# Optimization experiments

Measured on AMD Instinct MI355X. Metric: run time of the kernel, lower is better.

The kernel has to match this reference:

```python
import jax, jax.numpy as jnp
import numpy as np

N_NODES = 16384
N_EDGES = 8192
MAX_DEG = 32
IN_DIM = 128
EDGE_DIM = 64
N_HEADS = 8
OUT_DIM = 16
OUT_CH = N_HEADS * OUT_DIM  # 128 == IN_DIM -> residual is Identity


def setup_inputs() -> dict:
    key = jax.random.key(0)
    ks = jax.random.split(key, 16)
    # incidence matrix H [N, E]: each hyperedge touches up to MAX_DEG random nodes
    rng = np.random.default_rng(0)
    cols = rng.integers(0, N_NODES, size=(N_EDGES, MAX_DEG))
    H_np = np.zeros((N_NODES, N_EDGES), dtype=np.float32)
    H_np[cols, np.arange(N_EDGES)[:, None]] = 1.0  # duplicates collapse -> deg <= MAX_DEG
    s = 0.02
    return {
        "q": jax.random.normal(ks[0], (N_NODES, IN_DIM), jnp.float32),
        "k": jax.random.normal(ks[1], (N_NODES, IN_DIM), jnp.float32),
        "v": jax.random.normal(ks[2], (N_NODES, IN_DIM), jnp.float32),
        "edge_feat": jax.random.normal(ks[3], (N_NODES, EDGE_DIM), jnp.float32),
        "H": jnp.asarray(H_np),
        "Wq": jax.random.normal(ks[4], (IN_DIM, OUT_CH), jnp.float32) * s,
        "Wk": jax.random.normal(ks[5], (IN_DIM, OUT_CH), jnp.float32) * s,
        "Wv": jax.random.normal(ks[6], (IN_DIM, OUT_CH), jnp.float32) * s,
        "We": jax.random.normal(ks[7], (EDGE_DIM, N_HEADS), jnp.float32) * s,
        "be": jnp.zeros((N_HEADS,), jnp.float32),
        "Wo": jax.random.normal(ks[8], (OUT_CH, OUT_CH), jnp.float32) * s,
        "W1": jax.random.normal(ks[9], (OUT_CH, 2 * OUT_CH), jnp.float32) * s,
        "b1": jnp.zeros((2 * OUT_CH,), jnp.float32),
        "W2": jax.random.normal(ks[10], (2 * OUT_CH, OUT_CH), jnp.float32) * s,
        "b2": jnp.zeros((OUT_CH,), jnp.float32),
        "max_deg": MAX_DEG,
    }


def hgt_forward(q, k, v, edge_feat, H, Wq, Wk, Wv, We, be, Wo, W1, b1, W2, b2, max_deg):
    N = q.shape[0]
    E = H.shape[1]
    nH, C = be.shape[0], Wq.shape[1]
    d = C // nH
    scale = 1.0 / (d ** 0.5)

    qd = (q @ Wq).reshape(N, nH, d)
    ksrc = (k @ Wk).reshape(N, nH, d)
    vsrc = (v @ Wv).reshape(N, nH, d)

    Ht = H.T  # [E, N]
    # node indices of each hyperedge, padded to max_deg (stable argsort: ones first, ascending)
    idx = jnp.argsort(-Ht, axis=1)[:, :max_deg]            # [E, K]
    deg = jnp.sum(Ht, axis=1).astype(jnp.int32)            # [E]
    mask = jnp.arange(max_deg)[None, :] < deg[:, None]     # [E, K]

    q_pad = qd[idx]   # [E, K, nH, d]
    k_pad = ksrc[idx]
    score = jnp.sum(q_pad * k_pad, axis=-1) * scale        # [E, K, nH]

    # hyperedge features and ADD edge attention bias
    he_feat = Ht @ edge_feat                               # [E, edge_dim]
    edge_attn = he_feat @ We + be                          # [E, nH]
    score = score + edge_attn[:, None, :]

    # segment softmax over nodes (normalize each node's attention over its hyperedges)
    flat_idx = jnp.where(mask, idx, N).reshape(-1)         # invalid slots -> dummy segment N
    score_flat = jnp.where(mask[..., None], score, -jnp.inf).reshape(-1, nH)
    seg_max = jax.ops.segment_max(score_flat, flat_idx, num_segments=N + 1)[:N]  # [N, nH]
    exp_e = jnp.where(mask[..., None], jnp.exp(score - seg_max[idx]), 0.0)       # [E, K, nH]
    seg_sum = jax.ops.segment_sum(exp_e.reshape(-1, nH), flat_idx, num_segments=N + 1)[:N]
    attn = exp_e / (seg_sum[idx] + 1e-10)                  # [E, K, nH]; 0 at padded slots

    # messages and aggregation: rst = H @ sum_over_slots(attn * v)
    v_pad = vsrc[idx]                                      # [E, K, nH, d]
    msg_sum = jnp.sum((v_pad * attn[..., None]).reshape(E, max_deg, C), axis=1)  # [E, C]
    rst = H @ msg_sum                                      # [N, C]

    rst = rst @ Wo
    rst = rst + q                                          # residual (Identity: in_dim == out_channel)
    h = rst
    rst = jax.nn.relu(rst @ W1 + b1) @ W2 + b2             # FFN
    return rst + h                                         # second residual


def reference(q, k, v, edge_feat, H, Wq, Wk, Wv, We, be, Wo, W1, b1, W2, b2, max_deg):
    return hgt_forward(q, k, v, edge_feat, H, Wq, Wk, Wv, We, be, Wo, W1, b1, W2, b2, max_deg)
```

## Files before the change

kernel.cpp:

```cpp
#include <hip/hip_runtime.h>

#define N_NODES 16384
#define N_EDGES 8192
#define MAXD 32
#define NODE_CAP 64

#define GEMM_BLKS 512
#define PE_BLKS 256
#define CVT_BLKS 256

typedef __attribute__((ext_vector_type(8))) short bf16x8;
typedef __attribute__((ext_vector_type(4))) float f32x4;

__device__ __forceinline__ unsigned f2b(float f) {
    unsigned u = __float_as_uint(f);
    return (u + 0x7FFFu + ((u >> 16) & 1u)) >> 16;
}
__device__ __forceinline__ unsigned pack2(float lo, float hi) {
    return f2b(lo) | (f2b(hi) << 16);
}
__device__ __forceinline__ float blo(unsigned w) { return __uint_as_float(w << 16); }
__device__ __forceinline__ float bhi(unsigned w) { return __uint_as_float(w & 0xFFFF0000u); }

__device__ __forceinline__ int row_u4(uint4 x, int c4, int row, int base,
                                      int* __restrict__ node_edges, int lane)
{
    const unsigned* xs = (const unsigned*)&x;
#pragma unroll
    for (int k2 = 0; k2 < 4; ++k2) {
        unsigned long long m = __ballot(xs[k2] != 0u);
        if (xs[k2]) {
            int pos = base + (int)__popcll(m & ((1ull << lane) - 1ull));
            if (pos < NODE_CAP) node_edges[row * NODE_CAP + pos] = c4 * 4 + k2;
        }
        base += (int)__popcll(m);
    }
    return base;
}

__global__ __launch_bounds__(256, 8) void scan_rows_k(const float* __restrict__ H,
    int* __restrict__ node_cnt, int* __restrict__ node_edges)
{
    const int wid  = threadIdx.x >> 6;
    const int lane = threadIdx.x & 63;
    const int row  = blockIdx.x * 4 + wid;
    const uint4* Hr = (const uint4*)H + (size_t)row * 2048;
    int base = 0;
#pragma unroll 1
    for (int it = 0; it < 32; it += 4) {
        uint4 x0 = Hr[(it + 0) * 64 + lane];
        uint4 x1 = Hr[(it + 1) * 64 + lane];
        uint4 x2 = Hr[(it + 2) * 64 + lane];
        uint4 x3 = Hr[(it + 3) * 64 + lane];
        base = row_u4(x0, (it + 0) * 64 + lane, row, base, node_edges, lane);
        base = row_u4(x1, (it + 1) * 64 + lane, row, base, node_edges, lane);
        base = row_u4(x2, (it + 2) * 64 + lane, row, base, node_edges, lane);
        base = row_u4(x3, (it + 3) * 64 + lane, row, base, node_edges, lane);
    }
    if (lane == 0) node_cnt[row] = base;
}

__global__ __launch_bounds__(256) void build_k(const int* __restrict__ node_cnt,
    const int* __restrict__ node_edges, int* __restrict__ edge_cnt,
    int* __restrict__ edge_nodes)
{
    int idx = blockIdx.x * 256 + threadIdx.x;
    int n = idx >> 6, s = idx & 63;
    if (s < min(node_cnt[n], NODE_CAP)) {
        int e = node_edges[n * NODE_CAP + s];
        int p = atomicAdd(&edge_cnt[e], 1);
        if (p < MAXD) edge_nodes[e * MAXD + p] = n;
    }
}

__global__ __launch_bounds__(256) void vwe_k(
    const float* __restrict__ v, const float* __restrict__ Wv,
    const float* __restrict__ ef, const float* __restrict__ We,
    const float* __restrict__ W1, const float* __restrict__ W2,
    float* __restrict__ vsrc, float* __restrict__ pe,
    unsigned short* __restrict__ W1t, unsigned short* __restrict__ W2t)
{
    const int b = blockIdx.x, tid = threadIdx.x;
    if (b < GEMM_BLKS) {
        const int row0 = b * 32;
        const int r  = tid >> 4;
        const int c0 = (tid & 15) * 8;
        const float4* A4 = (const float4*)v;
        const float4* B4 = (const float4*)Wv;
        float acc[2][8];
#pragma unroll
        for (int i = 0; i < 2; ++i)
#pragma unroll
            for (int j = 0; j < 8; ++j) acc[i][j] = 0.f;
#pragma unroll 4
        for (int k4 = 0; k4 < 32; ++k4) {
            float4 a0 = A4[(size_t)(row0 + r) * 32 + k4];
            float4 a1 = A4[(size_t)(row0 + r + 16) * 32 + k4];
#pragma unroll
            for (int kk = 0; kk < 4; ++kk) {
                int k = k4 * 4 + kk;
                float4 b0 = B4[k * 32 + (c0 >> 2)];
                float4 b1 = B4[k * 32 + (c0 >> 2) + 1];
                float av0 = kk == 0 ? a0.x : kk == 1 ? a0.y : kk == 2 ? a0.z : a0.w;
                float av1 = kk == 0 ? a1.x : kk == 1 ? a1.y : kk == 2 ? a1.z : a1.w;
                acc[0][0] = fmaf(av0, b0.x, acc[0][0]); acc[0][1] = fmaf(av0, b0.y, acc[0][1]);
                acc[0][2] = fmaf(av0, b0.z, acc[0][2]); acc[0][3] = fmaf(av0, b0.w, acc[0][3]);
                acc[0][4] = fmaf(av0, b1.x, acc[0][4]); acc[0][5] = fmaf(av0, b1.y, acc[0][5]);
                acc[0][6] = fmaf(av0, b1.z, acc[0][6]); acc[0][7] = fmaf(av0, b1.w, acc[0][7]);
                acc[1][0] = fmaf(av1, b0.x, acc[1][0]); acc[1][1] = fmaf(av1, b0.y, acc[1][1]);
                acc[1][2] = fmaf(av1, b0.z, acc[1][2]); acc[1][3] = fmaf(av1, b0.w, acc[1][3]);
                acc[1][4] = fmaf(av1, b1.x, acc[1][4]); acc[1][5] = fmaf(av1, b1.y, acc[1][5]);
                acc[1][6] = fmaf(av1, b1.z, acc[1][6]); acc[1][7] = fmaf(av1, b1.w, acc[1][7]);
            }
        }
#pragma unroll
        for (int i = 0; i < 2; ++i) {
            int row = row0 + r + i * 16;
            float4 o0 = {acc[i][0], acc[i][1], acc[i][2], acc[i][3]};
            float4 o1 = {acc[i][4], acc[i][5], acc[i][6], acc[i][7]};
            *(float4*)&vsrc[(size_t)row * 128 + c0]     = o0;
            *(float4*)&vsrc[(size_t)row * 128 + c0 + 4] = o1;
        }
    } else if (b < GEMM_BLKS + PE_BLKS) {
        int base = (b - GEMM_BLKS) * 512 + tid;
#pragma unroll
        for (int t = 0; t < 2; ++t) {
            int g = base + t * 256;
            int n = g >> 3, h = g & 7;
            const float4* ef4 = (const float4*)ef + n * 16;
            float p = 0.f;
#pragma unroll
            for (int d4 = 0; d4 < 16; ++d4) {
                float4 x = ef4[d4];
                p += x.x * We[(d4 * 4 + 0) * 8 + h] + x.y * We[(d4 * 4 + 1) * 8 + h]
                   + x.z * We[(d4 * 4 + 2) * 8 + h] + x.w * We[(d4 * 4 + 3) * 8 + h];
            }
            pe[g] = p;
        }
    } else {
        int g2 = (b - GEMM_BLKS - PE_BLKS) * 256 + tid;
        if (g2 < 32768) {
            int n = g2 >> 7, k = g2 & 127;
            W1t[g2] = (unsigned short)f2b(W1[k * 256 + n]);
        } else {
            int g3 = g2 - 32768;
            int n = g3 >> 8, k = g3 & 255;
            W2t[g3] = (unsigned short)f2b(W2[k * 128 + n]);
        }
    }
}

__global__ __launch_bounds__(256) void eexp_k(const int* __restrict__ edge_cnt,
    const int* __restrict__ edge_nodes, const float* __restrict__ pe,
    const float* __restrict__ be, float* __restrict__ eexp)
{
    int g = blockIdx.x * 256 + threadIdx.x;
    int e = g >> 3, h = g & 7;
    int cnt = min(edge_cnt[e], MAXD);
    float s0 = be[h], s1 = 0.f, s2 = 0.f, s3 = 0.f;
    int j = 0;
    for (; j + 4 <= cnt; j += 4) {
        int4 nn = *(const int4*)&edge_nodes[e * MAXD + j];
        s0 += pe[nn.x * 8 + h];
        s1 += pe[nn.y * 8 + h];
        s2 += pe[nn.z * 8 + h];
        s3 += pe[nn.w * 8 + h];
    }
    for (; j < cnt; ++j) s0 += pe[edge_nodes[e * MAXD + j] * 8 + h];
    eexp[g] = __expf((s0 + s1) + (s2 + s3));
}

__global__ __launch_bounds__(256) void zu_k(const int* __restrict__ node_cnt,
    const int* __restrict__ node_edges, const float* __restrict__ eexp,
    const float* __restrict__ vsrc, uint4* __restrict__ u4)
{
    int g = blockIdx.x * 256 + threadIdx.x;
    int n = g >> 3, h = g & 7;
    int cnt = min(node_cnt[n], NODE_CAP);
    float z0 = 0.f, z1 = 0.f, z2 = 0.f, z3 = 0.f;
    int i = 0;
    for (; i + 4 <= cnt; i += 4) {
        int4 ee = *(const int4*)&node_edges[n * NODE_CAP + i];
        z0 += eexp[ee.x * 8 + h];
        z1 += eexp[ee.y * 8 + h];
        z2 += eexp[ee.z * 8 + h];
        z3 += eexp[ee.w * 8 + h];
    }
    for (; i < cnt; ++i) z0 += eexp[node_edges[n * NODE_CAP + i] * 8 + h];
    float s = 1.0f / (((z0 + z1) + (z2 + z3)) + 1e-10f);

    const float4* v4 = (const float4*)vsrc + (size_t)n * 32 + h * 4;
    float4 x0 = v4[0], x1 = v4[1], x2 = v4[2], x3 = v4[3];
    uint4 w0, w1;
    w0.x = pack2(s * x0.x, s * x0.y); w0.y = pack2(s * x0.z, s * x0.w);
    w0.z = pack2(s * x1.x, s * x1.y); w0.w = pack2(s * x1.z, s * x1.w);
    w1.x = pack2(s * x2.x, s * x2.y); w1.y = pack2(s * x2.z, s * x2.w);
    w1.z = pack2(s * x3.x, s * x3.y); w1.w = pack2(s * x3.z, s * x3.w);
    u4[(size_t)n * 16 + h * 2]     = w0;
    u4[(size_t)n * 16 + h * 2 + 1] = w1;
}

__global__ __launch_bounds__(256) void msgwo_k(const int* __restrict__ edge_cnt,
    const int* __restrict__ edge_nodes, const float* __restrict__ eexp,
    const uint4* __restrict__ u4, const float* __restrict__ Wo,
    uint4* __restrict__ msgo4)
{
    __shared__ float Ms[16][128];
    __shared__ float Bs[32][128];
    const int tid = threadIdx.x;
    const int e0  = blockIdx.x * 16;

    {
        int le = tid >> 4, c8 = tid & 15;
        int e = e0 + le;
        int h = c8 >> 1;
        int cnt = min(edge_cnt[e], MAXD);
        float eh = eexp[e * 8 + h];
        float a[8];
#pragma unroll
        for (int k = 0; k < 8; ++k) a[k] = 0.f;
        int j = 0;
        for (; j + 4 <= cnt; j += 4) {
            int4 nn = *(const int4*)&edge_nodes[e * MAXD + j];
            uint4 w0 = u4[(size_t)nn.x * 16 + c8];
            uint4 w1 = u4[(size_t)nn.y * 16 + c8];
            uint4 w2 = u4[(size_t)nn.z * 16 + c8];
            uint4 w3 = u4[(size_t)nn.w * 16 + c8];
            a[0] += (blo(w0.x) + blo(w1.x)) + (blo(w2.x) + blo(w3.x));
            a[1] += (bhi(w0.x) + bhi(w1.x)) + (bhi(w2.x) + bhi(w3.x));
            a[2] += (blo(w0.y) + blo(w1.y)) + (blo(w2.y) + blo(w3.y));
            a[3] += (bhi(w0.y) + bhi(w1.y)) + (bhi(w2.y) + bhi(w3.y));
            a[4] += (blo(w0.z) + blo(w1.z)) + (blo(w2.z) + blo(w3.z));
            a[5] += (bhi(w0.z) + bhi(w1.z)) + (bhi(w2.z) + bhi(w3.z));
            a[6] += (blo(w0.w) + blo(w1.w)) + (blo(w2.w) + blo(w3.w));
            a[7] += (bhi(w0.w) + bhi(w1.w)) + (bhi(w2.w) + bhi(w3.w));
        }
        for (; j < cnt; ++j) {
            uint4 w = u4[(size_t)edge_nodes[e * MAXD + j] * 16 + c8];
            a[0] += blo(w.x); a[1] += bhi(w.x); a[2] += blo(w.y); a[3] += bhi(w.y);
            a[4] += blo(w.z); a[5] += bhi(w.z); a[6] += blo(w.w); a[7] += bhi(w.w);
        }
        float4 o0 = {a[0]*eh, a[1]*eh, a[2]*eh, a[3]*eh};
        float4 o1 = {a[4]*eh, a[5]*eh, a[6]*eh, a[7]*eh};
        *(float4*)&Ms[le][c8 * 8]     = o0;
        *(float4*)&Ms[le][c8 * 8 + 4] = o1;
    }
    __syncthreads();

    const int r  = tid >> 4;
    const int c0 = (tid & 15) * 8;
    float acc[8];
#pragma unroll
    for (int j = 0; j < 8; ++j) acc[j] = 0.f;

    for (int kt = 0; kt < 128; kt += 32) {
#pragma unroll
        for (int u0 = 0; u0 < 4; ++u0) {
            int u = u0 * 256 + tid;
            int kk = u >> 5, cc = (u & 31) * 4;
            *(float4*)&Bs[kk][cc] = *(const float4*)&Wo[(kt + kk) * 128 + cc];
        }
        __syncthreads();
#pragma unroll
        for (int k = 0; k < 32; ++k) {
            float a = Ms[r][kt + k];
#pragma unroll
            for (int j = 0; j < 8; ++j)
                acc[j] = fmaf(a, Bs[k][c0 + j], acc[j]);
        }
        __syncthreads();
    }
    uint4 w;
    w.x = pack2(acc[0], acc[1]); w.y = pack2(acc[2], acc[3]);
    w.z = pack2(acc[4], acc[5]); w.w = pack2(acc[6], acc[7]);
    msgo4[(size_t)(e0 + r) * 16 + (c0 >> 3)] = w;
}

__global__ __launch_bounds__(256) void ffn_agg_k(const float* __restrict__ q,
    const int* __restrict__ node_cnt, const int* __restrict__ node_edges,
    const uint4* __restrict__ msgo4, const unsigned short* __restrict__ W1t,
    const float* __restrict__ b1, const unsigned short* __restrict__ W2t,
    const float* __restrict__ b2, float* __restrict__ out)
{
    __shared__ float Hs[32][128];
    __shared__ unsigned short Ha[32][128];
    __shared__ unsigned short Ta[32][256];

    const int tid  = threadIdx.x;
    const int row0 = blockIdx.x * 32;

    {
        int r = tid >> 3, lc = tid & 7;
        int n = row0 + r;
        const float4* q4 = (const float4*)q + (size_t)n * 32 + lc * 4;
        float a[16];
        {
            float4 qa = q4[0], qb = q4[1], qc = q4[2], qd = q4[3];
            a[0]=qa.x; a[1]=qa.y; a[2]=qa.z; a[3]=qa.w;
            a[4]=qb.x; a[5]=qb.y; a[6]=qb.z; a[7]=qb.w;
            a[8]=qc.x; a[9]=qc.y; a[10]=qc.z; a[11]=qc.w;
            a[12]=qd.x; a[13]=qd.y; a[14]=qd.z; a[15]=qd.w;
        }
        int cnt = min(node_cnt[n], NODE_CAP);
        int i = 0;
        for (; i + 2 <= cnt; i += 2) {
            int ea = node_edges[n * NODE_CAP + i];
            int eb = node_edges[n * NODE_CAP + i + 1];
            uint4 wa0 = msgo4[(size_t)ea * 16 + lc * 2];
            uint4 wa1 = msgo4[(size_t)ea * 16 + lc * 2 + 1];
            uint4 wb0 = msgo4[(size_t)eb * 16 + lc * 2];
            uint4 wb1 = msgo4[(size_t)eb * 16 + lc * 2 + 1];
            a[0]  += blo(wa0.x) + blo(wb0.x); a[1]  += bhi(wa0.x) + bhi(wb0.x);
            a[2]  += blo(wa0.y) + blo(wb0.y); a[3]  += bhi(wa0.y) + bhi(wb0.y);
            a[4]  += blo(wa0.z) + blo(wb0.z); a[5]  += bhi(wa0.z) + bhi(wb0.z);
            a[6]  += blo(wa0.w) + blo(wb0.w); a[7]  += bhi(wa0.w) + bhi(wb0.w);
            a[8]  += blo(wa1.x) + blo(wb1.x); a[9]  += bhi(wa1.x) + bhi(wb1.x);
            a[10] += blo(wa1.y) + blo(wb1.y); a[11] += bhi(wa1.y) + bhi(wb1.y);
            a[12] += blo(wa1.z) + blo(wb1.z); a[13] += bhi(wa1.z) + bhi(wb1.z);
            a[14] += blo(wa1.w) + blo(wb1.w); a[15] += bhi(wa1.w) + bhi(wb1.w);
        }
        for (; i < cnt; ++i) {
            int e = node_edges[n * NODE_CAP + i];
            uint4 w0 = msgo4[(size_t)e * 16 + lc * 2];
            uint4 w1 = msgo4[(size_t)e * 16 + lc * 2 + 1];
            a[0]  += blo(w0.x); a[1]  += bhi(w0.x); a[2]  += blo(w0.y); a[3]  += bhi(w0.y);
            a[4]  += blo(w0.z); a[5]  += bhi(w0.z); a[6]  += blo(w0.w); a[7]  += bhi(w0.w);
            a[8]  += blo(w1.x); a[9]  += bhi(w1.x); a[10] += blo(w1.y); a[11] += bhi(w1.y);
            a[12] += blo(w1.z); a[13] += bhi(w1.z); a[14] += blo(w1.w); a[15] += bhi(w1.w);
        }
#pragma unroll
        for (int k = 0; k < 4; ++k) {
            float4 o = {a[k*4+0], a[k*4+1], a[k*4+2], a[k*4+3]};
            *(float4*)&Hs[r][lc * 16 + k * 4] = o;
        }
#pragma unroll
        for (int t = 0; t < 8; ++t)
            *(unsigned*)&Ha[r][lc * 16 + 2 * t] = pack2(a[2*t], a[2*t+1]);
    }
    __syncthreads();

    const int wid  = tid >> 6;
    const int lane = tid & 63;
    const int lm = lane & 15;
    const int lk = (lane >> 4) * 8;
    const int lr = (lane >> 4) * 4;
    const int m  = wid & 1;

    {
        const int ng0 = (wid >> 1) * 8;
        f32x4 acc[8];
#pragma unroll
        for (int nt = 0; nt < 8; ++nt) acc[nt] = (f32x4){0.f, 0.f, 0.f, 0.f};
#pragma unroll
        for (int kt = 0; kt < 4; ++kt) {
            bf16x8 av = *(const bf16x8*)&Ha[m * 16 + lm][kt * 32 + lk];
#pragma unroll
            for (int nt = 0; nt < 8; ++nt) {
                bf16x8 bv = *(const bf16x8*)&W1t[(size_t)((ng0 + nt) * 16 + lm) * 128
                                                 + kt * 32 + lk];
                acc[nt] = __builtin_amdgcn_mfma_f32_16x16x32_bf16(av, bv, acc[nt], 0, 0, 0);
            }
        }
#pragma unroll
        for (int nt = 0; nt < 8; ++nt) {
            int col = (ng0 + nt) * 16 + lm;
            float bb = b1[col];
#pragma unroll
            for (int j = 0; j < 4; ++j) {
                float t = fmaxf(acc[nt][j] + bb, 0.f);
                Ta[m * 16 + lr + j][col] = (unsigned short)f2b(t);
            }
        }
    }
    __syncthreads();

    {
        const int ng0 = (wid >> 1) * 4;
        f32x4 acc[4];
#pragma unroll
        for (int nt = 0; nt < 4; ++nt) acc[nt] = (f32x4){0.f, 0.f, 0.f, 0.f};
#pragma unroll
        for (int kt = 0; kt < 8; ++kt) {
            bf16x8 av = *(const bf16x8*)&Ta[m * 16 + lm][kt * 32 + lk];
#pragma unroll
            for (int nt = 0; nt < 4; ++nt) {
                bf16x8 bv = *(const bf16x8*)&W2t[(size_t)((ng0 + nt) * 16 + lm) * 256
                                                 + kt * 32 + lk];
                acc[nt] = __builtin_amdgcn_mfma_f32_16x16x32_bf16(av, bv, acc[nt], 0, 0, 0);
            }
        }
#pragma unroll
        for (int nt = 0; nt < 4; ++nt) {
            int col = (ng0 + nt) * 16 + lm;
            float bb = b2[col];
#pragma unroll
            for (int j = 0; j < 4; ++j) {
                int rl = m * 16 + lr + j;
                out[(size_t)(row0 + rl) * 128 + col] = Hs[rl][col] + acc[nt][j] + bb;
            }
        }
    }
}

extern "C" void kernel_launch(void* const* d_in, const int* in_sizes, int n_in,
                              void* d_out, int out_size, void* d_ws, size_t ws_size,
                              hipStream_t stream)
{
    const float* q  = (const float*)d_in[0];
    const float* v  = (const float*)d_in[2];
    const float* ef = (const float*)d_in[3];
    const float* H  = (const float*)d_in[4];
    const float* Wv = (const float*)d_in[7];
    const float* We = (const float*)d_in[8];
    const float* be = (const float*)d_in[9];
    const float* Wo = (const float*)d_in[10];
    const float* W1 = (const float*)d_in[11];
    const float* b1 = (const float*)d_in[12];
    const float* W2 = (const float*)d_in[13];
    const float* b2 = (const float*)d_in[14];
    float* out = (float*)d_out;

    char* w = (char*)d_ws;
    auto carve = [&](size_t bytes) -> void* {
        void* p = (void*)w;
        w += (bytes + 255) & ~(size_t)255;
        return p;
    };
    int* edge_cnt   = (int*)carve(N_EDGES * 4);
    size_t zero_bytes = (size_t)(w - (char*)d_ws);
    int* node_cnt   = (int*)carve(N_NODES * 4);
    int* edge_nodes = (int*)carve((size_t)N_EDGES * MAXD * 4);
    int* node_edges = (int*)carve((size_t)N_NODES * NODE_CAP * 4);
    float* pe       = (float*)carve((size_t)N_NODES * 8 * 4);
    float* eexp     = (float*)carve((size_t)N_EDGES * 8 * 4);
    float* vsrc     = (float*)carve((size_t)N_NODES * 128 * 4);
    uint4* u4       = (uint4*)carve((size_t)N_NODES * 128 * 2);
    uint4* msgo4    = (uint4*)carve((size_t)N_EDGES * 128 * 2);
    unsigned short* W1t = (unsigned short*)carve(32768 * 2);
    unsigned short* W2t = (unsigned short*)carve(32768 * 2);
    (void)ws_size; (void)in_sizes; (void)n_in; (void)out_size;

    hipMemsetAsync(d_ws, 0, zero_bytes, stream);

    scan_rows_k<<<N_NODES / 4, 256, 0, stream>>>(H, node_cnt, node_edges);
    vwe_k<<<GEMM_BLKS + PE_BLKS + CVT_BLKS, 256, 0, stream>>>(v, Wv, ef, We, W1, W2,
                                                              vsrc, pe, W1t, W2t);
    build_k<<<(N_NODES * NODE_CAP) / 256, 256, 0, stream>>>(node_cnt, node_edges,
                                                            edge_cnt, edge_nodes);
    eexp_k<<<(N_EDGES * 8) / 256, 256, 0, stream>>>(edge_cnt, edge_nodes, pe, be, eexp);
    zu_k<<<(N_NODES * 8) / 256, 256, 0, stream>>>(node_cnt, node_edges, eexp, vsrc, u4);
    msgwo_k<<<N_EDGES / 16, 256, 0, stream>>>(edge_cnt, edge_nodes, eexp, u4, Wo, msgo4);
    ffn_agg_k<<<N_NODES / 32, 256, 0, stream>>>(q, node_cnt, node_edges, msgo4,
                                                W1t, b1, W2t, b2, out);
}
```

Measured before the change: 214.8 us.

## Move Wo projection from per-edge fp32 GEMM into node-side MFMA in FFN kernel

The Wo projection is no longer an fp32 shared-memory GEMM on edge messages inside the message kernel. It now runs as a bf16 MFMA on the aggregated node rows inside the FFN kernel, using a pre-transposed bf16 Wo, and the residual q is added afterwards. This uses linearity (H@(M Wo) = (H@M) Wo) to turn the message kernel into a pure gather-sum with more blocks, at the cost of doing the projection per node (twice as many rows) and quantizing to bf16 before Wo. The H row scan is also software-pipelined with double-buffered loads.

```diff
diff --git a/kernel.cpp b/kernel.cpp
--- a/kernel.cpp
+++ b/kernel.cpp
@@ -7,7 +7,7 @@
 
 #define GEMM_BLKS 512
 #define PE_BLKS 256
-#define CVT_BLKS 256
+#define CVT_BLKS 320
 
 typedef __attribute__((ext_vector_type(8))) short bf16x8;
 typedef __attribute__((ext_vector_type(4))) float f32x4;
@@ -46,16 +46,25 @@
     const int row  = blockIdx.x * 4 + wid;
     const uint4* Hr = (const uint4*)H + (size_t)row * 2048;
     int base = 0;
+    uint4 a0, a1, a2, a3, b0, b1, b2, b3;
+    a0 = Hr[0 * 64 + lane]; a1 = Hr[1 * 64 + lane];
+    a2 = Hr[2 * 64 + lane]; a3 = Hr[3 * 64 + lane];
 #pragma unroll 1
-    for (int it = 0; it < 32; it += 4) {
-        uint4 x0 = Hr[(it + 0) * 64 + lane];
-        uint4 x1 = Hr[(it + 1) * 64 + lane];
-        uint4 x2 = Hr[(it + 2) * 64 + lane];
-        uint4 x3 = Hr[(it + 3) * 64 + lane];
-        base = row_u4(x0, (it + 0) * 64 + lane, row, base, node_edges, lane);
-        base = row_u4(x1, (it + 1) * 64 + lane, row, base, node_edges, lane);
-        base = row_u4(x2, (it + 2) * 64 + lane, row, base, node_edges, lane);
-        base = row_u4(x3, (it + 3) * 64 + lane, row, base, node_edges, lane);
+    for (int it = 0; it < 32; it += 8) {
+        b0 = Hr[(it + 4) * 64 + lane]; b1 = Hr[(it + 5) * 64 + lane];
+        b2 = Hr[(it + 6) * 64 + lane]; b3 = Hr[(it + 7) * 64 + lane];
+        base = row_u4(a0, (it + 0) * 64 + lane, row, base, node_edges, lane);
+        base = row_u4(a1, (it + 1) * 64 + lane, row, base, node_edges, lane);
+        base = row_u4(a2, (it + 2) * 64 + lane, row, base, node_edges, lane);
+        base = row_u4(a3, (it + 3) * 64 + lane, row, base, node_edges, lane);
+        if (it + 8 < 32) {
+            a0 = Hr[(it +  8) * 64 + lane]; a1 = Hr[(it +  9) * 64 + lane];
+            a2 = Hr[(it + 10) * 64 + lane]; a3 = Hr[(it + 11) * 64 + lane];
+        }
+        base = row_u4(b0, (it + 4) * 64 + lane, row, base, node_edges, lane);
+        base = row_u4(b1, (it + 5) * 64 + lane, row, base, node_edges, lane);
+        base = row_u4(b2, (it + 6) * 64 + lane, row, base, node_edges, lane);
+        base = row_u4(b3, (it + 7) * 64 + lane, row, base, node_edges, lane);
     }
     if (lane == 0) node_cnt[row] = base;
 }
@@ -76,9 +85,11 @@
 __global__ __launch_bounds__(256) void vwe_k(
     const float* __restrict__ v, const float* __restrict__ Wv,
     const float* __restrict__ ef, const float* __restrict__ We,
-    const float* __restrict__ W1, const float* __restrict__ W2,
+    const float* __restrict__ Wo, const float* __restrict__ W1,
+    const float* __restrict__ W2,
     float* __restrict__ vsrc, float* __restrict__ pe,
-    unsigned short* __restrict__ W1t, unsigned short* __restrict__ W2t)
+    unsigned short* __restrict__ Wot, unsigned short* __restrict__ W1t,
+    unsigned short* __restrict__ W2t)
 {
     const int b = blockIdx.x, tid = threadIdx.x;
     if (b < GEMM_BLKS) {
@@ -142,10 +153,14 @@
         if (g2 < 32768) {
             int n = g2 >> 7, k = g2 & 127;
             W1t[g2] = (unsigned short)f2b(W1[k * 256 + n]);
-        } else {
+        } else if (g2 < 65536) {
             int g3 = g2 - 32768;
             int n = g3 >> 8, k = g3 & 255;
             W2t[g3] = (unsigned short)f2b(W2[k * 128 + n]);
+        } else {
+            int g4 = g2 - 65536;
+            int n = g4 >> 7, k = g4 & 127;
+            Wot[g4] = (unsigned short)f2b(Wo[k * 128 + n]);
         }
     }
 }
@@ -200,88 +215,52 @@
     u4[(size_t)n * 16 + h * 2 + 1] = w1;
 }
 
-__global__ __launch_bounds__(256) void msgwo_k(const int* __restrict__ edge_cnt,
+__global__ __launch_bounds__(256) void msg_k(const int* __restrict__ edge_cnt,
     const int* __restrict__ edge_nodes, const float* __restrict__ eexp,
-    const uint4* __restrict__ u4, const float* __restrict__ Wo,
-    uint4* __restrict__ msgo4)
-{
-    __shared__ float Ms[16][128];
-    __shared__ float Bs[32][128];
-    const int tid = threadIdx.x;
-    const int e0  = blockIdx.x * 16;
-
-    {
-        int le = tid >> 4, c8 = tid & 15;
-        int e = e0 + le;
-        int h = c8 >> 1;
-        int cnt = min(edge_cnt[e], MAXD);
-        float eh = eexp[e * 8 + h];
-        float a[8];
-#pragma unroll
-        for (int k = 0; k < 8; ++k) a[k] = 0.f;
-        int j = 0;
-        for (; j + 4 <= cnt; j += 4) {
-            int4 nn = *(const int4*)&edge_nodes[e * MAXD + j];
-            uint4 w0 = u4[(size_t)nn.x * 16 + c8];
-            uint4 w1 = u4[(size_t)nn.y * 16 + c8];
-            uint4 w2 = u4[(size_t)nn.z * 16 + c8];
-            uint4 w3 = u4[(size_t)nn.w * 16 + c8];
-            a[0] += (blo(w0.x) + blo(w1.x)) + (blo(w2.x) + blo(w3.x));
-            a[1] += (bhi(w0.x) + bhi(w1.x)) + (bhi(w2.x) + bhi(w3.x));
-            a[2] += (blo(w0.y) + blo(w1.y)) + (blo(w2.y) + blo(w3.y));
-            a[3] += (bhi(w0.y) + bhi(w1.y)) + (bhi(w2.y) + bhi(w3.y));
-            a[4] += (blo(w0.z) + blo(w1.z)) + (blo(w2.z) + blo(w3.z));
-            a[5] += (bhi(w0.z) + bhi(w1.z)) + (bhi(w2.z) + bhi(w3.z));
-            a[6] += (blo(w0.w) + blo(w1.w)) + (blo(w2.w) + blo(w3.w));
-            a[7] += (bhi(w0.w) + bhi(w1.w)) + (bhi(w2.w) + bhi(w3.w));
-        }
-        for (; j < cnt; ++j) {
-            uint4 w = u4[(size_t)edge_nodes[e * MAXD + j] * 16 + c8];
-            a[0] += blo(w.x); a[1] += bhi(w.x); a[2] += blo(w.y); a[3] += bhi(w.y);
-            a[4] += blo(w.z); a[5] += bhi(w.z); a[6] += blo(w.w); a[7] += bhi(w.w);
-        }
-        float4 o0 = {a[0]*eh, a[1]*eh, a[2]*eh, a[3]*eh};
-        float4 o1 = {a[4]*eh, a[5]*eh, a[6]*eh, a[7]*eh};
-        *(float4*)&Ms[le][c8 * 8]     = o0;
-        *(float4*)&Ms[le][c8 * 8 + 4] = o1;
-    }
-    __syncthreads();
-
-    const int r  = tid >> 4;
-    const int c0 = (tid & 15) * 8;
-    float acc[8];
-#pragma unroll
-    for (int j = 0; j < 8; ++j) acc[j] = 0.f;
-
-    for (int kt = 0; kt < 128; kt += 32) {
-#pragma unroll
-        for (int u0 = 0; u0 < 4; ++u0) {
-            int u = u0 * 256 + tid;
-            int kk = u >> 5, cc = (u & 31) * 4;
-            *(float4*)&Bs[kk][cc] = *(const float4*)&Wo[(kt + kk) * 128 + cc];
-        }
-        __syncthreads();
-#pragma unroll
-        for (int k = 0; k < 32; ++k) {
-            float a = Ms[r][kt + k];
-#pragma unroll
-            for (int j = 0; j < 8; ++j)
-                acc[j] = fmaf(a, Bs[k][c0 + j], acc[j]);
-        }
-        __syncthreads();
+    const uint4* __restrict__ u4, uint4* __restrict__ msg4)
+{
+    int g = blockIdx.x * 256 + threadIdx.x;
+    int e = g >> 4, c8 = g & 15, h = c8 >> 1;
+    int cnt = min(edge_cnt[e], MAXD);
+    float eh = eexp[e * 8 + h];
+    float a[8];
+#pragma unroll
+    for (int k = 0; k < 8; ++k) a[k] = 0.f;
+    int j = 0;
+    for (; j + 4 <= cnt; j += 4) {
+        int4 nn = *(const int4*)&edge_nodes[e * MAXD + j];
+        uint4 w0 = u4[(size_t)nn.x * 16 + c8];
+        uint4 w1 = u4[(size_t)nn.y * 16 + c8];
+        uint4 w2 = u4[(size_t)nn.z * 16 + c8];
+        uint4 w3 = u4[(size_t)nn.w * 16 + c8];
+        a[0] += (blo(w0.x) + blo(w1.x)) + (blo(w2.x) + blo(w3.x));
+        a[1] += (bhi(w0.x) + bhi(w1.x)) + (bhi(w2.x) + bhi(w3.x));
+        a[2] += (blo(w0.y) + blo(w1.y)) + (blo(w2.y) + blo(w3.y));
+        a[3] += (bhi(w0.y) + bhi(w1.y)) + (bhi(w2.y) + bhi(w3.y));
+        a[4] += (blo(w0.z) + blo(w1.z)) + (blo(w2.z) + blo(w3.z));
+        a[5] += (bhi(w0.z) + bhi(w1.z)) + (bhi(w2.z) + bhi(w3.z));
+        a[6] += (blo(w0.w) + blo(w1.w)) + (blo(w2.w) + blo(w3.w));
+        a[7] += (bhi(w0.w) + bhi(w1.w)) + (bhi(w2.w) + bhi(w3.w));
+    }
+    for (; j < cnt; ++j) {
+        uint4 w = u4[(size_t)edge_nodes[e * MAXD + j] * 16 + c8];
+        a[0] += blo(w.x); a[1] += bhi(w.x); a[2] += blo(w.y); a[3] += bhi(w.y);
+        a[4] += blo(w.z); a[5] += bhi(w.z); a[6] += blo(w.w); a[7] += bhi(w.w);
     }
     uint4 w;
-    w.x = pack2(acc[0], acc[1]); w.y = pack2(acc[2], acc[3]);
-    w.z = pack2(acc[4], acc[5]); w.w = pack2(acc[6], acc[7]);
-    msgo4[(size_t)(e0 + r) * 16 + (c0 >> 3)] = w;
+    w.x = pack2(a[0] * eh, a[1] * eh); w.y = pack2(a[2] * eh, a[3] * eh);
+    w.z = pack2(a[4] * eh, a[5] * eh); w.w = pack2(a[6] * eh, a[7] * eh);
+    msg4[g] = w;
 }
 
 __global__ __launch_bounds__(256) void ffn_agg_k(const float* __restrict__ q,
     const int* __restrict__ node_cnt, const int* __restrict__ node_edges,
-    const uint4* __restrict__ msgo4, const unsigned short* __restrict__ W1t,
-    const float* __restrict__ b1, const unsigned short* __restrict__ W2t,
-    const float* __restrict__ b2, float* __restrict__ out)
-{
+    const uint4* __restrict__ msg4, const unsigned short* __restrict__ Wot,
+    const unsigned short* __restrict__ W1t, const float* __restrict__ b1,
+    const unsigned short* __restrict__ W2t, const float* __restrict__ b2,
+    float* __restrict__ out)
+{
+    __shared__ unsigned short Ra[32][128];
     __shared__ float Hs[32][128];
     __shared__ unsigned short Ha[32][128];
     __shared__ unsigned short Ta[32][256];
@@ -292,24 +271,18 @@
     {
         int r = tid >> 3, lc = tid & 7;
         int n = row0 + r;
-        const float4* q4 = (const float4*)q + (size_t)n * 32 + lc * 4;
         float a[16];
-        {
-            float4 qa = q4[0], qb = q4[1], qc = q4[2], qd = q4[3];
-            a[0]=qa.x; a[1]=qa.y; a[2]=qa.z; a[3]=qa.w;
-            a[4]=qb.x; a[5]=qb.y; a[6]=qb.z; a[7]=qb.w;
-            a[8]=qc.x; a[9]=qc.y; a[10]=qc.z; a[11]=qc.w;
-            a[12]=qd.x; a[13]=qd.y; a[14]=qd.z; a[15]=qd.w;
-        }
+#pragma unroll
+        for (int k = 0; k < 16; ++k) a[k] = 0.f;
         int cnt = min(node_cnt[n], NODE_CAP);
         int i = 0;
         for (; i + 2 <= cnt; i += 2) {
             int ea = node_edges[n * NODE_CAP + i];
             int eb = node_edges[n * NODE_CAP + i + 1];
-            uint4 wa0 = msgo4[(size_t)ea * 16 + lc * 2];
-            uint4 wa1 = msgo4[(size_t)ea * 16 + lc * 2 + 1];
-            uint4 wb0 = msgo4[(size_t)eb * 16 + lc * 2];
-            uint4 wb1 = msgo4[(size_t)eb * 16 + lc * 2 + 1];
+            uint4 wa0 = msg4[(size_t)ea * 16 + lc * 2];
+            uint4 wa1 = msg4[(size_t)ea * 16 + lc * 2 + 1];
+            uint4 wb0 = msg4[(size_t)eb * 16 + lc * 2];
+            uint4 wb1 = msg4[(size_t)eb * 16 + lc * 2 + 1];
             a[0]  += blo(wa0.x) + blo(wb0.x); a[1]  += bhi(wa0.x) + bhi(wb0.x);
             a[2]  += blo(wa0.y) + blo(wb0.y); a[3]  += bhi(wa0.y) + bhi(wb0.y);
             a[4]  += blo(wa0.z) + blo(wb0.z); a[5]  += bhi(wa0.z) + bhi(wb0.z);
@@ -321,21 +294,16 @@
         }
         for (; i < cnt; ++i) {
             int e = node_edges[n * NODE_CAP + i];
-            uint4 w0 = msgo4[(size_t)e * 16 + lc * 2];
-            uint4 w1 = msgo4[(size_t)e * 16 + lc * 2 + 1];
+            uint4 w0 = msg4[(size_t)e * 16 + lc * 2];
+            uint4 w1 = msg4[(size_t)e * 16 + lc * 2 + 1];
             a[0]  += blo(w0.x); a[1]  += bhi(w0.x); a[2]  += blo(w0.y); a[3]  += bhi(w0.y);
             a[4]  += blo(w0.z); a[5]  += bhi(w0.z); a[6]  += blo(w0.w); a[7]  += bhi(w0.w);
             a[8]  += blo(w1.x); a[9]  += bhi(w1.x); a[10] += blo(w1.y); a[11] += bhi(w1.y);
             a[12] += blo(w1.z); a[13] += bhi(w1.z); a[14] += blo(w1.w); a[15] += bhi(w1.w);
         }
 #pragma unroll
-        for (int k = 0; k < 4; ++k) {
-            float4 o = {a[k*4+0], a[k*4+1], a[k*4+2], a[k*4+3]};
-            *(float4*)&Hs[r][lc * 16 + k * 4] = o;
-        }
-#pragma unroll
         for (int t = 0; t < 8; ++t)
-            *(unsigned*)&Ha[r][lc * 16 + 2 * t] = pack2(a[2*t], a[2*t+1]);
+            *(unsigned*)&Ra[r][lc * 16 + 2 * t] = pack2(a[2*t], a[2*t+1]);
     }
     __syncthreads();
 
@@ -345,6 +313,35 @@
     const int lk = (lane >> 4) * 8;
     const int lr = (lane >> 4) * 4;
     const int m  = wid & 1;
+
+    {
+        const int ng0 = (wid >> 1) * 4;
+        f32x4 acc[4];
+#pragma unroll
+        for (int nt = 0; nt < 4; ++nt) acc[nt] = (f32x4){0.f, 0.f, 0.f, 0.f};
+#pragma unroll
+        for (int kt = 0; kt < 4; ++kt) {
+            bf16x8 av = *(const bf16x8*)&Ra[m * 16 + lm][kt * 32 + lk];
+#pragma unroll
+            for (int nt = 0; nt < 4; ++nt) {
+                bf16x8 bv = *(const bf16x8*)&Wot[(size_t)((ng0 + nt) * 16 + lm) * 128
+                                                 + kt * 32 + lk];
+                acc[nt] = __builtin_amdgcn_mfma_f32_16x16x32_bf16(av, bv, acc[nt], 0, 0, 0);
+            }
+        }
+#pragma unroll
+        for (int nt = 0; nt < 4; ++nt) {
+            int col = (ng0 + nt) * 16 + lm;
+#pragma unroll
+            for (int j = 0; j < 4; ++j) {
+                int rl = m * 16 + lr + j;
+                float hv = acc[nt][j] + q[(size_t)(row0 + rl) * 128 + col];
+                Hs[rl][col] = hv;
+                Ha[rl][col] = (unsigned short)f2b(hv);
+            }
+        }
+    }
+    __syncthreads();
 
     {
         const int ng0 = (wid >> 1) * 8;
@@ -435,21 +432,22 @@
     float* eexp     = (float*)carve((size_t)N_EDGES * 8 * 4);
     float* vsrc     = (float*)carve((size_t)N_NODES * 128 * 4);
     uint4* u4       = (uint4*)carve((size_t)N_NODES * 128 * 2);
-    uint4* msgo4    = (uint4*)carve((size_t)N_EDGES * 128 * 2);
+    uint4* msg4     = (uint4*)carve((size_t)N_EDGES * 128 * 2);
     unsigned short* W1t = (unsigned short*)carve(32768 * 2);
     unsigned short* W2t = (unsigned short*)carve(32768 * 2);
+    unsigned short* Wot = (unsigned short*)carve(16384 * 2);
     (void)ws_size; (void)in_sizes; (void)n_in; (void)out_size;
 
     hipMemsetAsync(d_ws, 0, zero_bytes, stream);
 
     scan_rows_k<<<N_NODES / 4, 256, 0, stream>>>(H, node_cnt, node_edges);
-    vwe_k<<<GEMM_BLKS + PE_BLKS + CVT_BLKS, 256, 0, stream>>>(v, Wv, ef, We, W1, W2,
-                                                              vsrc, pe, W1t, W2t);
+    vwe_k<<<GEMM_BLKS + PE_BLKS + CVT_BLKS, 256, 0, stream>>>(v, Wv, ef, We, Wo, W1, W2,
+                                                              vsrc, pe, Wot, W1t, W2t);
     build_k<<<(N_NODES * NODE_CAP) / 256, 256, 0, stream>>>(node_cnt, node_edges,
                                                             edge_cnt, edge_nodes);
     eexp_k<<<(N_EDGES * 8) / 256, 256, 0, stream>>>(edge_cnt, edge_nodes, pe, be, eexp);
     zu_k<<<(N_NODES * 8) / 256, 256, 0, stream>>>(node_cnt, node_edges, eexp, vsrc, u4);
-    msgwo_k<<<N_EDGES / 16, 256, 0, stream>>>(edge_cnt, edge_nodes, eexp, u4, Wo, msgo4);
-    ffn_agg_k<<<N_NODES / 32, 256, 0, stream>>>(q, node_cnt, node_edges, msgo4,
-                                                W1t, b1, W2t, b2, out);
-}
+    msg_k<<<(N_EDGES * 16) / 256, 256, 0, stream>>>(edge_cnt, edge_nodes, eexp, u4, msg4);
+    ffn_agg_k<<<N_NODES / 32, 256, 0, stream>>>(q, node_cnt, node_edges, msg4,
+                                                Wot, W1t, b1, W2t, b2, out);
+}
```

Measured after the change: 207.8 us (median of 2 runs). 3.2% less time.
